# Performance work log

Hardware: AMD Instinct MI355X
Metric: run time of the kernel (lower is better)

Reference implementation:

```python
import jax, jax.numpy as jnp
import numpy as np

HID = 64        # HIDDEN_DIM
SLOTS = 6       # MEMORY_SLOTS
V = 64          # VOCAB_SIZE
NH = 2          # attention heads
THRESH = 0.5    # STAGE1_THRESH
EPS = 1e-5      # LayerNorm eps (torch default)


def setup_inputs() -> dict:
    key = jax.random.key(0)
    ks = jax.random.split(key, 16)
    B, L = 64, 1024
    def n(k, shape, s=0.05):
        return jax.random.normal(k, shape, jnp.float32) * s
    return {
        'seq':    jax.random.randint(ks[0], (B, L), 0, V),
        'query':  jax.random.randint(ks[1], (B,), 0, V),
        'target': jax.random.randint(ks[2], (B,), 0, V),
        # TinyEncoder params
        'embed':   n(ks[3], (V, HID)),
        'wqkv':    n(ks[4], (3 * HID, HID)), 'bqkv': jnp.zeros(3 * HID, jnp.float32),
        'wo_attn': n(ks[5], (HID, HID)),     'bo_attn': jnp.zeros(HID, jnp.float32),
        'w_ff1':   n(ks[6], (2 * HID, HID)), 'b_ff1': jnp.zeros(2 * HID, jnp.float32),
        'w_ff2':   n(ks[7], (HID, 2 * HID)), 'b_ff2': jnp.zeros(HID, jnp.float32),
        'g1': jnp.ones(HID, jnp.float32), 'be1': jnp.zeros(HID, jnp.float32),
        'g2': jnp.ones(HID, jnp.float32), 'be2': jnp.zeros(HID, jnp.float32),
        # gates
        'w_s1': n(ks[8], (1, HID)), 'b_s1': jnp.zeros(1, jnp.float32),
        'w_s2': n(ks[9], (1, HID)), 'b_s2': jnp.zeros(1, jnp.float32),
        # MemoryReader
        'w_qr': n(ks[10], (HID, HID)), 'b_qr': jnp.zeros(HID, jnp.float32),
        'w_or': n(ks[11], (V, HID)),   'b_or': jnp.zeros(V, jnp.float32),
        # query embedding
        'q_embed': n(ks[12], (V, HID)),
    }


def _layernorm(x, g, b):
    m = x.mean(-1, keepdims=True)
    v = ((x - m) ** 2).mean(-1, keepdims=True)
    return (x - m) * jax.lax.rsqrt(v + EPS) * g + b


def _mha(h, wqkv, bqkv, wo, bo):
    B, L, H = h.shape
    d = H // NH
    qkv = h @ wqkv.T + bqkv                      # [B,L,3H]
    q, k, v = jnp.split(qkv, 3, axis=-1)
    q = q.reshape(B, L, NH, d)
    k = k.reshape(B, L, NH, d)
    v = v.reshape(B, L, NH, d)
    scores = jnp.einsum('bqhd,bkhd->bhqk', q, k) / jnp.sqrt(jnp.float32(d))
    w = jax.nn.softmax(scores, axis=-1)          # [B,NH,L,L]
    o = jnp.einsum('bhqk,bkhd->bqhd', w, v).reshape(B, L, H)
    return o @ wo.T + bo


def reference(seq, query, target, embed, wqkv, bqkv, wo_attn, bo_attn,
              w_ff1, b_ff1, w_ff2, b_ff2, g1, be1, g2, be2,
              w_s1, b_s1, w_s2, b_s2, w_qr, b_qr, w_or, b_or, q_embed):
    # --- TinyEncoder ---
    h = embed[seq]                                           # [B,L,H]
    a = _mha(h, wqkv, bqkv, wo_attn, bo_attn)
    h = _layernorm(h + a, g1, be1)
    ff = jax.nn.relu(h @ w_ff1.T + b_ff1) @ w_ff2.T + b_ff2
    hidden = _layernorm(h + ff, g2, be2)                     # [B,L,H]

    # --- two-stage selection (vectorized; dead s1-branch elided) ---
    s1 = jax.nn.sigmoid(jnp.squeeze(hidden @ w_s1.T + b_s1, -1))   # [B,L]
    keep = (s1 > THRESH).astype(hidden.dtype)
    s2 = jax.nn.sigmoid(jnp.squeeze(hidden @ w_s2.T + b_s2, -1))
    s2f = s2 * keep
    _, topk = jax.lax.top_k(s2f, SLOTS)                            # [B,SLOTS]

    # --- gather memory slots ---
    mem = jnp.take_along_axis(hidden, topk[:, :, None], axis=1)    # [B,SLOTS,H]

    # --- MemoryReader ---
    q_h = q_embed[query]                                           # [B,H]
    q = q_h @ w_qr.T + b_qr                                        # [B,H]
    scores = (q[:, None, :] * mem).sum(-1) / jnp.sqrt(jnp.float32(HID))  # [B,SLOTS]
    w = jax.nn.softmax(scores, axis=-1)
    ctx = (w[:, :, None] * mem).sum(1)                             # [B,H]
    logits = ctx @ w_or.T + b_or                                   # [B,V]

    # --- cross entropy (mean) ---
    logp = jax.nn.log_softmax(logits, axis=-1)
    loss = -jnp.take_along_axis(logp, target[:, None], axis=1).mean()
    return loss
```

## Files before the change

### kernel.cpp

```cpp
#include <hip/hip_runtime.h>

#define DEV __device__ __forceinline__

DEV int   f2i(float v){ return __builtin_bit_cast(int, v); }
DEV float i2f(int v){ return __builtin_bit_cast(float, v); }
DEV float blane(float v, int l){ return i2f(__builtin_amdgcn_readlane(f2i(v), l)); }

template<int C, int RM> DEV float dpp_add_m(float v){
  return v + i2f(__builtin_amdgcn_update_dpp(0, f2i(v), C, RM, 0xF, true));
}
template<int C, int RM> DEV float dpp_max_m(float v){
  return fmaxf(v, i2f(__builtin_amdgcn_update_dpp(0, f2i(v), C, RM, 0xF, true)));
}
DEV float wred_sum(float v){
  v = dpp_add_m<0xB1,0xF>(v); v = dpp_add_m<0x4E,0xF>(v);
  v = dpp_add_m<0x141,0xF>(v); v = dpp_add_m<0x140,0xF>(v);
  v = dpp_add_m<0x142,0xA>(v);
  v = dpp_add_m<0x143,0xC>(v);
  return blane(v, 63);
}
DEV float wred_max(float v){
  v = dpp_max_m<0xB1,0xF>(v); v = dpp_max_m<0x4E,0xF>(v);
  v = dpp_max_m<0x141,0xF>(v); v = dpp_max_m<0x140,0xF>(v);
  v = dpp_max_m<0x142,0xA>(v);
  v = dpp_max_m<0x143,0xC>(v);
  return blane(v, 63);
}

DEV float wsum(float v){
  #pragma unroll
  for (int o = 32; o; o >>= 1) v += __shfl_xor(v, o, 64);
  return v;
}
DEV float wmax(float v){
  #pragma unroll
  for (int o = 32; o; o >>= 1) v = fmaxf(v, __shfl_xor(v, o, 64));
  return v;
}

__global__ __launch_bounds__(1024) void k_prep(
    const int* __restrict__ seq, const float* __restrict__ embed,
    const float* __restrict__ wqkv, const float* __restrict__ bqkv,
    float* __restrict__ qkv_tab, float* __restrict__ cnt_f,
    float* __restrict__ out){
  const int b = blockIdx.x, tid = threadIdx.x;
  if (b == 0 && tid == 0) out[0] = 0.f;
  __shared__ float emb[64];
  __shared__ int hh[64];
  if (tid < 64){ emb[tid] = embed[b*64 + tid]; hh[tid] = 0; }
  __syncthreads();
  atomicAdd(&hh[seq[b*1024 + tid]], 1);
  if (tid < 192){
    const float4* w4 = (const float4*)(wqkv + tid*64);
    float a0 = bqkv[tid], a1 = 0.f, a2 = 0.f, a3 = 0.f;
    #pragma unroll
    for (int k = 0; k < 16; k += 4){
      float4 wa = w4[k],   wb = w4[k+1], wc = w4[k+2], wd = w4[k+3];
      a0 += wa.x*emb[4*k]    + wa.y*emb[4*k+1]  + wa.z*emb[4*k+2]  + wa.w*emb[4*k+3];
      a1 += wb.x*emb[4*k+4]  + wb.y*emb[4*k+5]  + wb.z*emb[4*k+6]  + wb.w*emb[4*k+7];
      a2 += wc.x*emb[4*k+8]  + wc.y*emb[4*k+9]  + wc.z*emb[4*k+10] + wc.w*emb[4*k+11];
      a3 += wd.x*emb[4*k+12] + wd.y*emb[4*k+13] + wd.z*emb[4*k+14] + wd.w*emb[4*k+15];
    }
    qkv_tab[b*192 + tid] = (a0+a1)+(a2+a3);
  }
  __syncthreads();
  if (tid < 64) cnt_f[b*64 + tid] = (float)hh[tid];
}

__global__ __launch_bounds__(512, 4) void k_attn(
    const float* __restrict__ qkv_tab, const float* __restrict__ cnt_f,
    const float* __restrict__ embed,
    const float* __restrict__ wo_attn, const float* __restrict__ bo_attn,
    const float* __restrict__ g1, const float* __restrict__ be1,
    float* __restrict__ xn_tab){
  const int b = blockIdx.x >> 3, oct = blockIdx.x & 7;
  const int tid = threadIdx.x, w = tid >> 6, lane = tid & 63;

  __shared__ float4 k4 [64*16];
  __shared__ float4 v4t[64*16];
  __shared__ float4 wo4[64*16];
  __shared__ float  cnt_lds[64];

  const float4* qkv4 = (const float4*)qkv_tab;
  const float4* wo_4 = (const float4*)wo_attn;
  float* v4f = (float*)v4t;

  #pragma unroll
  for (int ii = 0; ii < 2; ++ii){
    int i = tid + ii*512;
    int r = i >> 4, c4 = i & 15, s = c4 ^ (r & 15);
    k4 [r*16 + s] = qkv4[r*48 + 16 + c4];
    wo4[r*16 + s] = wo_4[i];
    float4 vv = qkv4[r*48 + 32 + c4];
    int d0 = 4*c4;
    v4f[(d0  )*64 + 4*((r>>2) ^ ((d0  )&15)) + (r&3)] = vv.x;
    v4f[(d0+1)*64 + 4*((r>>2) ^ ((d0+1)&15)) + (r&3)] = vv.y;
    v4f[(d0+2)*64 + 4*((r>>2) ^ ((d0+2)&15)) + (r&3)] = vv.z;
    v4f[(d0+3)*64 + 4*((r>>2) ^ ((d0+3)&15)) + (r&3)] = vv.w;
  }
  if (tid < 64) cnt_lds[tid] = cnt_f[b*64 + tid];
  __syncthreads();

  const int   tok = oct*8 + w;
  const int   sw = lane & 15;
  const float cme  = cnt_lds[lane];
  const bool  pres = cme > 0.f;
  const float sc = 0.17677669529663687f;
  const float g1v = g1[lane], be1v = be1[lane];
  const float bov = bo_attn[lane];

  float q0 = qkv_tab[tok*192 + lane];
  float sA = 0.f, sB = 0.f;
  #pragma unroll
  for (int c4 = 0; c4 < 16; ++c4){
    float4 kk = k4[lane*16 + (c4 ^ sw)];
    #pragma unroll
    for (int j = 0; j < 4; ++j){
      const int d = 4*c4 + j;
      float ke = (j==0)?kk.x:(j==1)?kk.y:(j==2)?kk.z:kk.w;
      float b0 = blane(q0, d);
      if (d < 32) sA += b0*ke; else sB += b0*ke;
    }
  }
  float s0 = sA*sc, s1 = sB*sc;
  float m0 = wred_max(pres ? s0 : -1e30f);
  float m1 = wred_max(pres ? s1 : -1e30f);
  float p0 = pres ? cme*__expf(s0 - m0) : 0.f;
  float p1 = pres ? cme*__expf(s1 - m1) : 0.f;
  float d0v = wred_sum(p0);
  float d1v = wred_sum(p1);
  float o = 0.f;
  #pragma unroll
  for (int c4 = 0; c4 < 16; ++c4){
    float4 vv = v4t[lane*16 + (c4 ^ sw)];
    #pragma unroll
    for (int j = 0; j < 4; ++j){
      const int tp = 4*c4 + j;
      float ve = (j==0)?vv.x:(j==1)?vv.y:(j==2)?vv.z:vv.w;
      float a0 = blane(p0, tp), a1 = blane(p1, tp);
      o += (lane < 32 ? a0 : a1) * ve;
    }
  }
  o /= (lane < 32 ? d0v : d1v);
  float aT = bov;
  #pragma unroll
  for (int c4 = 0; c4 < 16; ++c4){
    float4 ww = wo4[lane*16 + (c4 ^ sw)];
    #pragma unroll
    for (int j = 0; j < 4; ++j){
      const int k = 4*c4 + j;
      float we = (j==0)?ww.x:(j==1)?ww.y:(j==2)?ww.z:ww.w;
      aT += we*blane(o, k);
    }
  }
  float x = embed[tok*64 + lane] + aT;
  float mu = wred_sum(x) * 0.015625f;
  float xm = x - mu;
  float var = wred_sum(xm*xm) * 0.015625f;
  float xn = xm * rsqrtf(var + 1e-5f) * g1v + be1v;
  xn_tab[(b*64 + tok)*64 + lane] = xn;
}

__global__ __launch_bounds__(512, 4) void k_ffn(
    const float* __restrict__ xn_tab,
    const float* __restrict__ w_ff1, const float* __restrict__ b_ff1,
    const float* __restrict__ w_ff2, const float* __restrict__ b_ff2,
    const float* __restrict__ g2, const float* __restrict__ be2,
    const float* __restrict__ w_s1, const float* __restrict__ b_s1,
    const float* __restrict__ w_s2, const float* __restrict__ b_s2,
    float* __restrict__ hidden_tab, float* __restrict__ s2f_tab){
  const int b = blockIdx.x >> 3, oct = blockIdx.x & 7;
  const int tid = threadIdx.x, w = tid >> 6, lane = tid & 63;

  __shared__ float4 f14[128*16];
  __shared__ float4 f24[64*32];

  const float4* f1_4 = (const float4*)w_ff1;
  const float4* f2_4 = (const float4*)w_ff2;

  #pragma unroll
  for (int ii = 0; ii < 4; ++ii){
    int i = tid + ii*512;
    int r1 = i >> 4, c41 = i & 15;
    f14[r1*16 + (c41 ^ (r1 & 15))] = f1_4[i];
    int r2 = i >> 5, c42 = i & 31;
    f24[r2*32 + (c42 ^ (r2 & 15))] = f2_4[i];
  }
  __syncthreads();

  const int   tok = oct*8 + w;
  const int   sw = lane & 15;
  const float g2v = g2[lane], be2v = be2[lane];
  const float bf2v = b_ff2[lane];
  const float bf1a = b_ff1[lane], bf1b = b_ff1[64 + lane];
  const float ws1v = w_s1[lane], ws2v = w_s2[lane];
  const float bs1 = b_s1[0], bs2 = b_s2[0];

  float xn = xn_tab[(b*64 + tok)*64 + lane];
  float y0 = bf1a, y1 = bf1b;
  #pragma unroll
  for (int c4 = 0; c4 < 16; ++c4){
    float4 wA = f14[lane*16 + (c4 ^ sw)];
    float4 wB = f14[(lane+64)*16 + (c4 ^ sw)];
    #pragma unroll
    for (int j = 0; j < 4; ++j){
      const int k = 4*c4 + j;
      float wa = (j==0)?wA.x:(j==1)?wA.y:(j==2)?wA.z:wA.w;
      float wb = (j==0)?wB.x:(j==1)?wB.y:(j==2)?wB.z:wB.w;
      float x0 = blane(xn, k);
      y0 += wa*x0;
      y1 += wb*x0;
    }
  }
  y0 = fmaxf(y0, 0.f); y1 = fmaxf(y1, 0.f);
  float z = bf2v;
  #pragma unroll
  for (int c4 = 0; c4 < 32; ++c4){
    float4 ww = f24[lane*32 + (c4 ^ sw)];
    #pragma unroll
    for (int j = 0; j < 4; ++j){
      const int jj = 4*c4 + j;
      float we = (j==0)?ww.x:(j==1)?ww.y:(j==2)?ww.z:ww.w;
      if (jj < 64) z += we*blane(y0, jj);
      else         z += we*blane(y1, jj-64);
    }
  }
  float r = xn + z;
  float mu2 = wred_sum(r) * 0.015625f;
  float rm = r - mu2;
  float var2 = wred_sum(rm*rm) * 0.015625f;
  float hid = rm * rsqrtf(var2 + 1e-5f) * g2v + be2v;
  float t1 = wred_sum(hid * ws1v) + bs1;
  float t2 = wred_sum(hid * ws2v) + bs2;
  float sg1 = 1.f / (1.f + __expf(-t1));
  float sg2 = 1.f / (1.f + __expf(-t2));
  float s2f = (sg1 > 0.5f) ? sg2 : 0.f;
  hidden_tab[(b*64 + tok)*64 + lane] = hid;
  if (lane == 0) s2f_tab[b*64 + tok] = s2f;
}

__global__ __launch_bounds__(256) void k_sel(
    const int* __restrict__ seq, const int* __restrict__ query,
    const int* __restrict__ target,
    const float* __restrict__ hidden_tab, const float* __restrict__ s2f_tab,
    const float* __restrict__ w_qr, const float* __restrict__ b_qr,
    const float* __restrict__ w_or, const float* __restrict__ b_or,
    const float* __restrict__ q_embed, float* __restrict__ out){
  const int b = blockIdx.x, tid = threadIdx.x, lane = tid & 63, jr = tid >> 6;
  __shared__ float s2_lds[64];
  __shared__ float wq_lds[64*65];
  __shared__ float wor_lds[64*65];
  if (tid < 64) s2_lds[tid] = s2f_tab[b*64 + tid];
  #pragma unroll
  for (int j0 = 0; j0 < 16; ++j0){
    int j = j0*4 + jr;
    wq_lds[j*65 + lane]  = w_qr[j*64 + lane];
    wor_lds[j*65 + lane] = w_or[j*64 + lane];
  }
  __syncthreads();
  if (tid >= 64) return;

  float vals[16];
  #pragma unroll
  for (int j = 0; j < 16; ++j){
    int tk = seq[b*1024 + j*64 + lane];
    vals[j] = s2_lds[tk];
  }
  int sel[6];
  #pragma unroll
  for (int r = 0; r < 6; ++r){
    float bv = -1.f; int bi = 1 << 30;
    #pragma unroll
    for (int j = 0; j < 16; ++j){
      float v = vals[j]; int i = (j << 6) | lane;
      if (v > bv || (v == bv && i < bi)){ bv = v; bi = i; }
    }
    #pragma unroll
    for (int o = 32; o; o >>= 1){
      float ov = __shfl_xor(bv, o, 64);
      int   oi = __shfl_xor(bi, o, 64);
      if (ov > bv || (ov == bv && oi < bi)){ bv = ov; bi = oi; }
    }
    sel[r] = bi;
    int jw = bi >> 6, lw = bi & 63;
    if (lane == lw){
      #pragma unroll
      for (int j = 0; j < 16; ++j) if (j == jw) vals[j] = -1.f;
    }
  }

  float mem[6];
  #pragma unroll
  for (int s = 0; s < 6; ++s){
    int tk = seq[b*1024 + sel[s]];
    mem[s] = hidden_tab[(b*64 + tk)*64 + lane];
  }
  float qe = q_embed[query[b]*64 + lane];
  float qv0 = b_qr[lane], qv1 = 0.f, qv2 = 0.f, qv3 = 0.f;
  #pragma unroll
  for (int k = 0; k < 64; k += 4){
    qv0 += wq_lds[lane*65 + k]     * __shfl(qe, k, 64);
    qv1 += wq_lds[lane*65 + k + 1] * __shfl(qe, k+1, 64);
    qv2 += wq_lds[lane*65 + k + 2] * __shfl(qe, k+2, 64);
    qv3 += wq_lds[lane*65 + k + 3] * __shfl(qe, k+3, 64);
  }
  float qv = (qv0 + qv1) + (qv2 + qv3);
  float scv[6];
  #pragma unroll
  for (int s = 0; s < 6; ++s) scv[s] = wsum(qv * mem[s]) * 0.125f;
  float mx = scv[0];
  #pragma unroll
  for (int s = 1; s < 6; ++s) mx = fmaxf(mx, scv[s]);
  float e[6], se = 0.f;
  #pragma unroll
  for (int s = 0; s < 6; ++s){ e[s] = __expf(scv[s] - mx); se += e[s]; }
  float ctx = 0.f;
  #pragma unroll
  for (int s = 0; s < 6; ++s) ctx += (e[s] / se) * mem[s];
  float l0 = b_or[lane], l1 = 0.f, l2 = 0.f, l3 = 0.f;
  #pragma unroll
  for (int k = 0; k < 64; k += 4){
    l0 += wor_lds[lane*65 + k]     * __shfl(ctx, k, 64);
    l1 += wor_lds[lane*65 + k + 1] * __shfl(ctx, k+1, 64);
    l2 += wor_lds[lane*65 + k + 2] * __shfl(ctx, k+2, 64);
    l3 += wor_lds[lane*65 + k + 3] * __shfl(ctx, k+3, 64);
  }
  float lg = (l0 + l1) + (l2 + l3);
  float lm = wmax(lg);
  float ss = wsum(__expf(lg - lm));
  float lt = __shfl(lg, target[b], 64);
  if (lane == 0) atomicAdd(out, -(lt - lm - __logf(ss)) * 0.015625f);
}

extern "C" void kernel_launch(void* const* d_in, const int* in_sizes, int n_in,
                              void* d_out, int out_size, void* d_ws, size_t ws_size,
                              hipStream_t stream){
  const int*   seq     = (const int*)  d_in[0];
  const int*   query   = (const int*)  d_in[1];
  const int*   target  = (const int*)  d_in[2];
  const float* embed   = (const float*)d_in[3];
  const float* wqkv    = (const float*)d_in[4];
  const float* bqkv    = (const float*)d_in[5];
  const float* wo_attn = (const float*)d_in[6];
  const float* bo_attn = (const float*)d_in[7];
  const float* w_ff1   = (const float*)d_in[8];
  const float* b_ff1   = (const float*)d_in[9];
  const float* w_ff2   = (const float*)d_in[10];
  const float* b_ff2   = (const float*)d_in[11];
  const float* g1      = (const float*)d_in[12];
  const float* be1     = (const float*)d_in[13];
  const float* g2      = (const float*)d_in[14];
  const float* be2     = (const float*)d_in[15];
  const float* w_s1    = (const float*)d_in[16];
  const float* b_s1    = (const float*)d_in[17];
  const float* w_s2    = (const float*)d_in[18];
  const float* b_s2    = (const float*)d_in[19];
  const float* w_qr    = (const float*)d_in[20];
  const float* b_qr    = (const float*)d_in[21];
  const float* w_or    = (const float*)d_in[22];
  const float* b_or    = (const float*)d_in[23];
  const float* q_embed = (const float*)d_in[24];

  float* ws = (float*)d_ws;
  float* qkv_tab    = ws;
  float* cnt_f      = ws + 12288;
  float* hidden_tab = ws + 16384;
  float* s2f_tab    = ws + 278528;
  float* xn_tab     = ws + 282624;

  float* out = (float*)d_out;

  k_prep<<<64, 1024, 0, stream>>>(seq, embed, wqkv, bqkv, qkv_tab, cnt_f, out);
  k_attn<<<512, 512, 0, stream>>>(qkv_tab, cnt_f, embed, wo_attn, bo_attn,
                                  g1, be1, xn_tab);
  k_ffn<<<512, 512, 0, stream>>>(xn_tab, w_ff1, b_ff1, w_ff2, b_ff2,
                                 g2, be2, w_s1, b_s1, w_s2, b_s2,
                                 hidden_tab, s2f_tab);
  k_sel<<<64, 256, 0, stream>>>(seq, query, target, hidden_tab, s2f_tab,
                                w_qr, b_qr, w_or, b_or, q_embed, out);
}
```

Measured before the change: 131.0 us.

## Precompute batch-independent attention score exponentials in a separate kernel

The query-key scores depend only on the vocabulary tokens, not the batch. A new k_score kernel computes the per-head exp(s - max) table once, and k_attn now only applies the per-batch count weighting and normalizes. This drops the redundant QK dot products, the K staging in shared memory and the masked max reductions from every attention block. The attention and FFN loops also gain split accumulators for more instruction-level parallelism, and global loads are moved ahead of the barrier. The cost is an extra kernel launch plus a small workspace table, and the max is now taken over all keys rather than only present ones.

```diff
diff --git a/kernel.cpp b/kernel.cpp
--- a/kernel.cpp
+++ b/kernel.cpp
@@ -67,20 +67,49 @@
   if (tid < 64) cnt_f[b*64 + tid] = (float)hh[tid];
 }
 
+__global__ __launch_bounds__(128) void k_score(
+    const float* __restrict__ qkv_tab, float* __restrict__ exp_tab){
+  const int t = blockIdx.x;
+  const int tid = threadIdx.x, h = tid >> 6, lane = tid & 63;
+  __shared__ float k_lds[64*65];
+  __shared__ float q_lds[64];
+  #pragma unroll
+  for (int ii = 0; ii < 32; ++ii){
+    int i = tid + ii*128;
+    k_lds[(i>>6)*65 + (i&63)] = qkv_tab[(i>>6)*192 + 64 + (i&63)];
+  }
+  if (tid < 64) q_lds[tid] = qkv_tab[t*192 + tid];
+  __syncthreads();
+  const float sc = 0.17677669529663687f;
+  float s0 = 0.f, s1 = 0.f;
+  #pragma unroll
+  for (int d = 0; d < 32; d += 2){
+    s0 += q_lds[h*32 + d]     * k_lds[lane*65 + h*32 + d];
+    s1 += q_lds[h*32 + d + 1] * k_lds[lane*65 + h*32 + d + 1];
+  }
+  float s = (s0 + s1) * sc;
+  float m = wred_max(s);
+  exp_tab[h*4096 + t*64 + lane] = __expf(s - m);
+}
+
 __global__ __launch_bounds__(512, 4) void k_attn(
     const float* __restrict__ qkv_tab, const float* __restrict__ cnt_f,
-    const float* __restrict__ embed,
+    const float* __restrict__ exp_tab, const float* __restrict__ embed,
     const float* __restrict__ wo_attn, const float* __restrict__ bo_attn,
     const float* __restrict__ g1, const float* __restrict__ be1,
     float* __restrict__ xn_tab){
   const int b = blockIdx.x >> 3, oct = blockIdx.x & 7;
   const int tid = threadIdx.x, w = tid >> 6, lane = tid & 63;
-
-  __shared__ float4 k4 [64*16];
+  const int tok = oct*8 + w;
+
+  const float cme  = cnt_f[b*64 + lane];
+  const float e0   = exp_tab[tok*64 + lane];
+  const float e1   = exp_tab[4096 + tok*64 + lane];
+  const float emb  = embed[tok*64 + lane];
+  const float g1v  = g1[lane], be1v = be1[lane], bov = bo_attn[lane];
+
   __shared__ float4 v4t[64*16];
   __shared__ float4 wo4[64*16];
-  __shared__ float  cnt_lds[64];
-
   const float4* qkv4 = (const float4*)qkv_tab;
   const float4* wo_4 = (const float4*)wo_attn;
   float* v4f = (float*)v4t;
@@ -89,7 +118,6 @@
   for (int ii = 0; ii < 2; ++ii){
     int i = tid + ii*512;
     int r = i >> 4, c4 = i & 15, s = c4 ^ (r & 15);
-    k4 [r*16 + s] = qkv4[r*48 + 16 + c4];
     wo4[r*16 + s] = wo_4[i];
     float4 vv = qkv4[r*48 + 32 + c4];
     int d0 = 4*c4;
@@ -98,62 +126,46 @@
     v4f[(d0+2)*64 + 4*((r>>2) ^ ((d0+2)&15)) + (r&3)] = vv.z;
     v4f[(d0+3)*64 + 4*((r>>2) ^ ((d0+3)&15)) + (r&3)] = vv.w;
   }
-  if (tid < 64) cnt_lds[tid] = cnt_f[b*64 + tid];
-  __syncthreads();
-
-  const int   tok = oct*8 + w;
-  const int   sw = lane & 15;
-  const float cme  = cnt_lds[lane];
-  const bool  pres = cme > 0.f;
-  const float sc = 0.17677669529663687f;
-  const float g1v = g1[lane], be1v = be1[lane];
-  const float bov = bo_attn[lane];
-
-  float q0 = qkv_tab[tok*192 + lane];
-  float sA = 0.f, sB = 0.f;
-  #pragma unroll
-  for (int c4 = 0; c4 < 16; ++c4){
-    float4 kk = k4[lane*16 + (c4 ^ sw)];
-    #pragma unroll
-    for (int j = 0; j < 4; ++j){
-      const int d = 4*c4 + j;
-      float ke = (j==0)?kk.x:(j==1)?kk.y:(j==2)?kk.z:kk.w;
-      float b0 = blane(q0, d);
-      if (d < 32) sA += b0*ke; else sB += b0*ke;
-    }
-  }
-  float s0 = sA*sc, s1 = sB*sc;
-  float m0 = wred_max(pres ? s0 : -1e30f);
-  float m1 = wred_max(pres ? s1 : -1e30f);
-  float p0 = pres ? cme*__expf(s0 - m0) : 0.f;
-  float p1 = pres ? cme*__expf(s1 - m1) : 0.f;
+  __syncthreads();
+
+  const int sw = lane & 15;
+  float p0 = cme * e0;
+  float p1 = cme * e1;
   float d0v = wred_sum(p0);
   float d1v = wred_sum(p1);
-  float o = 0.f;
-  #pragma unroll
-  for (int c4 = 0; c4 < 16; ++c4){
-    float4 vv = v4t[lane*16 + (c4 ^ sw)];
+  float oA = 0.f, oB = 0.f;
+  #pragma unroll
+  for (int c4 = 0; c4 < 16; c4 += 2){
+    float4 va = v4t[lane*16 + (c4 ^ sw)];
+    float4 vb = v4t[lane*16 + ((c4+1) ^ sw)];
     #pragma unroll
     for (int j = 0; j < 4; ++j){
-      const int tp = 4*c4 + j;
-      float ve = (j==0)?vv.x:(j==1)?vv.y:(j==2)?vv.z:vv.w;
-      float a0 = blane(p0, tp), a1 = blane(p1, tp);
-      o += (lane < 32 ? a0 : a1) * ve;
-    }
-  }
-  o /= (lane < 32 ? d0v : d1v);
-  float aT = bov;
-  #pragma unroll
-  for (int c4 = 0; c4 < 16; ++c4){
-    float4 ww = wo4[lane*16 + (c4 ^ sw)];
+      const int ta = 4*c4 + j, tb = ta + 4;
+      float vea = (j==0)?va.x:(j==1)?va.y:(j==2)?va.z:va.w;
+      float veb = (j==0)?vb.x:(j==1)?vb.y:(j==2)?vb.z:vb.w;
+      float a0 = blane(p0, ta), a1 = blane(p1, ta);
+      float b0 = blane(p0, tb), b1 = blane(p1, tb);
+      oA += (lane < 32 ? a0 : a1) * vea;
+      oB += (lane < 32 ? b0 : b1) * veb;
+    }
+  }
+  float o = (oA + oB) / (lane < 32 ? d0v : d1v);
+  float aT0 = bov, aT1 = 0.f;
+  #pragma unroll
+  for (int c4 = 0; c4 < 16; c4 += 2){
+    float4 wa = wo4[lane*16 + (c4 ^ sw)];
+    float4 wb = wo4[lane*16 + ((c4+1) ^ sw)];
     #pragma unroll
     for (int j = 0; j < 4; ++j){
-      const int k = 4*c4 + j;
-      float we = (j==0)?ww.x:(j==1)?ww.y:(j==2)?ww.z:ww.w;
-      aT += we*blane(o, k);
-    }
-  }
-  float x = embed[tok*64 + lane] + aT;
+      const int ka = 4*c4 + j, kb = ka + 4;
+      float wea = (j==0)?wa.x:(j==1)?wa.y:(j==2)?wa.z:wa.w;
+      float web = (j==0)?wb.x:(j==1)?wb.y:(j==2)?wb.z:wb.w;
+      aT0 += wea*blane(o, ka);
+      aT1 += web*blane(o, kb);
+    }
+  }
+  float aT = aT0 + aT1;
+  float x = emb + aT;
   float mu = wred_sum(x) * 0.015625f;
   float xm = x - mu;
   float var = wred_sum(xm*xm) * 0.015625f;
@@ -171,10 +183,17 @@
     float* __restrict__ hidden_tab, float* __restrict__ s2f_tab){
   const int b = blockIdx.x >> 3, oct = blockIdx.x & 7;
   const int tid = threadIdx.x, w = tid >> 6, lane = tid & 63;
+  const int tok = oct*8 + w;
+
+  const float xn   = xn_tab[(b*64 + tok)*64 + lane];
+  const float g2v  = g2[lane], be2v = be2[lane];
+  const float bf2v = b_ff2[lane];
+  const float bf1a = b_ff1[lane], bf1b = b_ff1[64 + lane];
+  const float ws1v = w_s1[lane], ws2v = w_s2[lane];
+  const float bs1  = b_s1[0], bs2 = b_s2[0];
 
   __shared__ float4 f14[128*16];
   __shared__ float4 f24[64*32];
-
   const float4* f1_4 = (const float4*)w_ff1;
   const float4* f2_4 = (const float4*)w_ff2;
 
@@ -188,43 +207,46 @@
   }
   __syncthreads();
 
-  const int   tok = oct*8 + w;
-  const int   sw = lane & 15;
-  const float g2v = g2[lane], be2v = be2[lane];
-  const float bf2v = b_ff2[lane];
-  const float bf1a = b_ff1[lane], bf1b = b_ff1[64 + lane];
-  const float ws1v = w_s1[lane], ws2v = w_s2[lane];
-  const float bs1 = b_s1[0], bs2 = b_s2[0];
-
-  float xn = xn_tab[(b*64 + tok)*64 + lane];
-  float y0 = bf1a, y1 = bf1b;
-  #pragma unroll
-  for (int c4 = 0; c4 < 16; ++c4){
-    float4 wA = f14[lane*16 + (c4 ^ sw)];
-    float4 wB = f14[(lane+64)*16 + (c4 ^ sw)];
+  const int sw = lane & 15;
+  float y0a = bf1a, y0b = 0.f, y1a = bf1b, y1b = 0.f;
+  #pragma unroll
+  for (int c4 = 0; c4 < 16; c4 += 2){
+    float4 wA0 = f14[lane*16 + (c4 ^ sw)];
+    float4 wA1 = f14[lane*16 + ((c4+1) ^ sw)];
+    float4 wB0 = f14[(lane+64)*16 + (c4 ^ sw)];
+    float4 wB1 = f14[(lane+64)*16 + ((c4+1) ^ sw)];
     #pragma unroll
     for (int j = 0; j < 4; ++j){
-      const int k = 4*c4 + j;
-      float wa = (j==0)?wA.x:(j==1)?wA.y:(j==2)?wA.z:wA.w;
-      float wb = (j==0)?wB.x:(j==1)?wB.y:(j==2)?wB.z:wB.w;
-      float x0 = blane(xn, k);
-      y0 += wa*x0;
-      y1 += wb*x0;
-    }
-  }
-  y0 = fmaxf(y0, 0.f); y1 = fmaxf(y1, 0.f);
-  float z = bf2v;
-  #pragma unroll
-  for (int c4 = 0; c4 < 32; ++c4){
-    float4 ww = f24[lane*32 + (c4 ^ sw)];
-    #pragma unroll
-    for (int j = 0; j < 4; ++j){
-      const int jj = 4*c4 + j;
-      float we = (j==0)?ww.x:(j==1)?ww.y:(j==2)?ww.z:ww.w;
-      if (jj < 64) z += we*blane(y0, jj);
-      else         z += we*blane(y1, jj-64);
-    }
-  }
+      const int ka = 4*c4 + j, kb = ka + 4;
+      float xa = blane(xn, ka), xb = blane(xn, kb);
+      float wa0 = (j==0)?wA0.x:(j==1)?wA0.y:(j==2)?wA0.z:wA0.w;
+      float wa1 = (j==0)?wA1.x:(j==1)?wA1.y:(j==2)?wA1.z:wA1.w;
+      float wb0 = (j==0)?wB0.x:(j==1)?wB0.y:(j==2)?wB0.z:wB0.w;
+      float wb1 = (j==0)?wB1.x:(j==1)?wB1.y:(j==2)?wB1.z:wB1.w;
+      y0a += wa0*xa; y0b += wa1*xb;
+      y1a += wb0*xa; y1b += wb1*xb;
+    }
+  }
+  float y0 = fmaxf(y0a + y0b, 0.f), y1 = fmaxf(y1a + y1b, 0.f);
+  float z0 = bf2v, z1 = 0.f, z2 = 0.f, z3 = 0.f;
+  #pragma unroll
+  for (int c4 = 0; c4 < 32; c4 += 4){
+    #pragma unroll
+    for (int u = 0; u < 4; ++u){
+      float4 ww = f24[lane*32 + ((c4+u) ^ sw)];
+      #pragma unroll
+      for (int j = 0; j < 4; ++j){
+        const int jj = 4*(c4+u) + j;
+        float we = (j==0)?ww.x:(j==1)?ww.y:(j==2)?ww.z:ww.w;
+        float yb = (jj < 64) ? blane(y0, jj) : blane(y1, jj-64);
+        if (u == 0) z0 += we*yb;
+        else if (u == 1) z1 += we*yb;
+        else if (u == 2) z2 += we*yb;
+        else z3 += we*yb;
+      }
+    }
+  }
+  float z = (z0 + z1) + (z2 + z3);
   float r = xn + z;
   float mu2 = wred_sum(r) * 0.015625f;
   float rm = r - mu2;
@@ -367,12 +389,14 @@
   float* hidden_tab = ws + 16384;
   float* s2f_tab    = ws + 278528;
   float* xn_tab     = ws + 282624;
+  float* exp_tab    = ws + 544768;
 
   float* out = (float*)d_out;
 
   k_prep<<<64, 1024, 0, stream>>>(seq, embed, wqkv, bqkv, qkv_tab, cnt_f, out);
-  k_attn<<<512, 512, 0, stream>>>(qkv_tab, cnt_f, embed, wo_attn, bo_attn,
-                                  g1, be1, xn_tab);
+  k_score<<<64, 128, 0, stream>>>(qkv_tab, exp_tab);
+  k_attn<<<512, 512, 0, stream>>>(qkv_tab, cnt_f, exp_tab, embed,
+                                  wo_attn, bo_attn, g1, be1, xn_tab);
   k_ffn<<<512, 512, 0, stream>>>(xn_tab, w_ff1, b_ff1, w_ff2, b_ff2,
                                  g2, be2, w_s1, b_s1, w_s2, b_s2,
                                  hidden_tab, s2f_tab);
```

Measured after the change: 131.6 us. Within noise of the previous version (+0.5%).
